# Optimization experiments

Measured on AMD Instinct MI355X. Metric: run time of the kernel, lower is better.

Reference implementation:

```python
import jax, jax.numpy as jnp
import numpy as np

ROT = 8
EPS = 1e-5


def _rot_offsets(ks, r):
    # integer-rounded rotated kernel tap offsets, exactly as cal_rot_pad
    c = (ks - 1) / 2
    locx = np.array([[j - c for j in range(ks)] for _ in range(ks)])
    locy = np.array([[i - c for _ in range(ks)] for i in range(ks)])
    loc = np.concatenate((locx.reshape(-1, 1), locy.reshape(-1, 1)), axis=1)  # [ks*ks, (x,y)]
    offs = []
    for i in range(r):
        th = 2.0 * np.pi / r * i
        R = np.array([[np.cos(th), -np.sin(th)], [np.sin(th), np.cos(th)]])
        offs.append(np.around(loc @ R).astype(np.int64))
    m = int(max(int(o.max()) for o in offs))
    return offs, m


def _build_rot_kernel(w, offs, m, r, separate):
    # w: [oc_r, cin, ks, ks]. The torch per-angle pad+cat+1x1conv+crop equals a
    # zero-padded (2m+1)x(2m+1) conv whose kernel scatters w[o,row,col,cin] at
    # (m - y_rot, m - x_rot), accumulating rounding collisions. Non-separate
    # layers cyclically roll the r input-channel blocks by the rotation index.
    oc_r, cin, ks, _ = w.shape
    K = 2 * m + 1
    kers = []
    for i in range(r):
        if separate:
            wi = w
        else:
            wb = w.reshape(oc_r, r, cin // r, ks, ks)
            wi = jnp.roll(wb, i, axis=1).reshape(oc_r, cin, ks, ks)
        wflat = wi.reshape(oc_r, cin, ks * ks)  # row-major tap order matches offs
        l = offs[i]
        ker = jnp.zeros((oc_r, cin, K, K), w.dtype)
        ker = ker.at[:, :, m - l[:, 1], m - l[:, 0]].add(wflat)
        kers.append(ker)
    return jnp.concatenate(kers, axis=0)  # rotation-major out channels, like torch.cat


def _conv(x, w, pad):
    return jax.lax.conv_general_dilated(
        x, w, (1, 1), [(pad, pad), (pad, pad)],
        dimension_numbers=('NCHW', 'OIHW', 'NCHW'))


def _rot_bn(x, gamma, beta, r):
    # training-mode BN applied independently to each rotation chunk, shared params
    B, C, H, W = x.shape
    xs = x.reshape(B, r, C // r, H, W)
    mu = xs.mean(axis=(0, 3, 4), keepdims=True)
    var = xs.var(axis=(0, 3, 4), keepdims=True)
    xn = (xs - mu) * jax.lax.rsqrt(var + EPS)
    xn = xn * gamma[None, None, :, None, None] + beta[None, None, :, None, None]
    return xn.reshape(B, C, H, W)


def _bn(x, gamma, beta):
    mu = x.mean(axis=(0, 2, 3), keepdims=True)
    var = x.var(axis=(0, 2, 3), keepdims=True)
    return (x - mu) * jax.lax.rsqrt(var + EPS) * gamma[None, :, None, None] + beta[None, :, None, None]


def _max_pool(x, k, pad=0):
    return jax.lax.reduce_window(
        x, -jnp.inf, jax.lax.max, (1, 1, k, k), (1, 1, k, k),
        [(0, 0), (0, 0), (pad, pad), (pad, pad)])


def _nms(x, r):
    # note: view is [B, C/r, r, H, W] (rotation-minor), exactly as the torch code
    B, C, H, W = x.shape
    xs = x.reshape(B, C // r, r, H, W)
    y = jnp.max(xs, axis=2, keepdims=True)
    mask = (y != xs).astype(x.dtype)
    return jnp.mean(xs * mask)


def _forward(x, w1, g1, b1, w2, g2, b2, w3, g3, b3,
             w4, g4, b4, w5, g5, b5, w6, g6, b6, w7, b7):
    offs, m = _rot_offsets(3, ROT)  # m == 1 for 3x3
    out = _conv(x, _build_rot_kernel(w1, offs, m, ROT, True), m)
    out = jax.nn.relu(_rot_bn(out, g1, b1, ROT))
    out = _conv(out, _build_rot_kernel(w2, offs, m, ROT, False), m)
    out = jax.nn.relu(_rot_bn(out, g2, b2, ROT))
    out = _max_pool(out, 2)
    out = _conv(out, _build_rot_kernel(w3, offs, m, ROT, False), m)
    out = jax.nn.relu(_rot_bn(out, g3, b3, ROT))
    n = _nms(out, ROT)
    out = jax.nn.relu(_bn(_conv(out, w4, 1), g4, b4))
    out = _max_pool(out, 2)
    out = jax.nn.relu(_bn(_conv(out, w5, 1), g5, b5))
    out = jax.nn.relu(_bn(_conv(out, w6, 1), g6, b6))
    out = _max_pool(out, 2, pad=1)
    out = _conv(out, w7, 2) + b7[None, :, None, None]
    out = _max_pool(out, out.shape[2])  # global max pool
    return out.reshape(out.shape[0], -1), n


def setup_inputs():
    key = jax.random.key(0)
    ks = jax.random.split(key, 24)
    f = jnp.float32
    d = {}
    d['x'] = jax.random.normal(ks[0], (2048, 1, 28, 28), f)
    wshapes = {'w1': (2, 1, 3, 3), 'w2': (2, 16, 3, 3), 'w3': (4, 16, 3, 3),
               'w4': (32, 32, 3, 3), 'w5': (64, 32, 3, 3), 'w6': (64, 64, 3, 3),
               'w7': (10, 64, 4, 4)}
    i = 1
    for name, sh in wshapes.items():
        d[name] = jax.random.normal(ks[i], sh, f) * 0.05
        i += 1
    bnc = {'1': 2, '2': 2, '3': 4, '4': 32, '5': 64, '6': 64}
    for suf, c in bnc.items():
        d['g' + suf] = 1.0 + 0.1 * jax.random.normal(ks[i], (c,), f)
        d['b' + suf] = 0.1 * jax.random.normal(ks[i + 1], (c,), f)
        i += 2
    d['b7'] = 0.1 * jax.random.normal(ks[i], (10,), f)
    return d


def reference(x, w1, w2, w3, w4, w5, w6, w7, g1, b1, g2, b2, g3, b3,
              g4, b4, g5, b5, g6, b6, b7):
    return _forward(x, w1, g1, b1, w2, g2, b2, w3, g3, b3,
                    w4, g4, b4, w5, g5, b5, w6, g6, b6, w7, b7)
```

## Files before the change

### kernel.cpp

```cpp
#include <hip/hip_runtime.h>

static constexpr int NB = 2048;
static constexpr float SENT = -1e30f;

typedef __attribute__((ext_vector_type(8))) short bf16x8;
typedef __attribute__((ext_vector_type(8))) unsigned short u16x8;
typedef __attribute__((ext_vector_type(4))) float f32x4;

#define ST_ADDR(base, ch, kind, copy) ((base) + (((ch)*4 + (copy))*32 + (kind)*8))

static constexpr int DST[8][9] = {
  {8,7,6,5,4,3,2,1,0},
  {5,8,7,2,4,6,1,0,3},
  {2,5,8,1,4,7,0,3,6},
  {1,2,5,0,4,8,3,6,7},
  {0,1,2,3,4,5,6,7,8},
  {3,0,1,6,4,2,7,8,5},
  {6,3,0,7,4,1,8,5,2},
  {7,6,3,8,4,0,5,2,1},
};

__device__ __forceinline__ unsigned short f2bf(float f){
  unsigned int u = __float_as_uint(f);
  u += 0x7fffu + ((u>>16)&1u);
  return (unsigned short)(u>>16);
}

__device__ __forceinline__ float bf2f(unsigned short h){
  return __uint_as_float((unsigned int)h << 16);
}

__device__ __forceinline__ unsigned int cvtpk(float lo, float hi){
  unsigned int r;
  asm("v_cvt_pk_bf16_f32 %0, %1, %2" : "=v"(r) : "v"(lo), "v"(hi));
  return r;
}

__device__ __forceinline__ unsigned int bnpair(unsigned int w, float a0, float b0, float a1, float b1){
  float vlo = __uint_as_float(w << 16);
  float vhi = __uint_as_float(w & 0xFFFF0000u);
  float r0 = fmaxf(vlo*a0 + b0, 0.f);
  float r1 = fmaxf(vhi*a1 + b1, 0.f);
  return cvtpk(r0, r1);
}

__device__ __forceinline__ float st_read(const float* base, int ch, int kind){
  return base[((ch*4+0)*32 + kind*8)] + base[((ch*4+1)*32 + kind*8)]
       + base[((ch*4+2)*32 + kind*8)] + base[((ch*4+3)*32 + kind*8)];
}

__device__ __forceinline__ int border_cell(int t){
  if (t<16) return t;
  if (t<32) return 240 + (t-16);
  if (t<46) return (t-31)*16;
  return (t-45)*16 + 15;
}

__global__ __launch_bounds__(256) void k_pre(const float* __restrict__ x, const float* __restrict__ w1,
                                             const float* __restrict__ w2, const float* __restrict__ w3,
                                             const float* __restrict__ w4,
                                             const float* __restrict__ w5, const float* __restrict__ w6,
                                             const float* __restrict__ w7,
                                             unsigned short* __restrict__ B2,
                                             unsigned short* __restrict__ B3,
                                             unsigned short* __restrict__ wb4,
                                             unsigned short* __restrict__ wb5, unsigned short* __restrict__ wb6,
                                             unsigned short* __restrict__ Bl,
                                             float* __restrict__ st){
  int blk = blockIdx.x;
  if (blk < 283){
    int i = blk*256 + threadIdx.x;
    if (i < 18432){
      int tap = i/2048, rem = i%2048, oc = rem/32, ci = rem%32;
      wb5[i] = f2bf(w5[(oc*32+ci)*9 + tap]);
    } else if (i < 55296){
      int j = i - 18432;
      int tap = j/4096, rem = j%4096, oc = rem/64, ci = rem%64;
      wb6[j] = f2bf(w6[(oc*64+ci)*9 + tap]);
    } else if (i < 64512){
      int j = i - 55296;
      int tap = j/1024, rem = j%1024, oc = rem/32, ci = rem%32;
      wb4[j] = f2bf(w4[(oc*32+ci)*9 + tap]);
    } else if (i < 67072){
      int j = i - 64512;
      int c = j >> 9;
      int rem = j & 511;
      int o = rem >> 5, k = rem & 31;
      int tap = c*2 + (k>>4);
      int ci = k & 15;
      unsigned short v = 0;
      if (tap <= 8){
        int rot = o>>1, u = o&1;
        int bb = ci>>1, ui = ci&1;
        int wc = (((bb - rot) & 7)<<1) | ui;
        int kk = 0;
        #pragma unroll
        for (int q=0;q<9;q++) if (DST[rot][q]==tap) kk=q;
        v = f2bf(w2[(u*16+wc)*9 + kk]);
      }
      B2[j] = v;
    } else if (i < 72192){
      int j = i - 67072;
      int c = j >> 10;
      int rem = j & 1023;
      int o = rem >> 5, k = rem & 31;
      int tap = c*2 + (k>>4);
      int ci = k & 15;
      unsigned short v = 0;
      if (tap <= 8){
        int rot = o>>2, uh = (o>>1)&1, ul = o&1;
        int bb = ci>>1, ui = ci&1;
        int wc = (((bb - rot) & 7)<<1) | ui;
        int kk = 0;
        #pragma unroll
        for (int q=0;q<9;q++) if (DST[rot][q]==tap) kk=q;
        v = f2bf(w3[uh*288 + (ul*16+wc)*9 + kk]);
      }
      B3[j] = v;
    }
    return;
  }
  if (blk < 1307){
    int i = (blk-283)*256 + threadIdx.x;
    int n = i>>10, k = i&1023;
    int pos16 = k>>6, ci = k&63;
    int r = pos16>>2, c = pos16&3;
    unsigned short v = 0;
    if (n < 250){
      int pos = n/10, o = n - 10*(n/10);
      int py = pos/5, px = pos - 5*(pos/5);
      int ky = r - py + 2, kx = c - px + 2;
      if (ky>=0 && ky<4 && kx>=0 && kx<4) v = f2bf(w7[(o*64+ci)*16 + ky*4 + kx]);
    }
    Bl[i] = v;
    return;
  }
  __shared__ float red[4][32];
  float wa[18];
  #pragma unroll
  for (int i=0;i<18;i++) wa[i] = w1[i];
  float s[16], s2[16];
  #pragma unroll
  for (int o=0;o<16;o++){ s[o]=0.f; s2[o]=0.f; }
  for (int idx = (blk-1307)*256 + threadIdx.x; idx < NB*784; idx += 512*256){
    int b = idx/784, pix = idx-b*784;
    int py = pix/28, px = pix-py*28;
    const float* xb = x + (size_t)b*784;
    float tap[9];
    #pragma unroll
    for (int d=0; d<9; d++){
      int dy = d/3-1, dx = d%3-1;
      int yy = py+dy, xx = px+dx;
      tap[d] = (yy>=0 && yy<28 && xx>=0 && xx<28) ? xb[yy*28+xx] : 0.f;
    }
    #pragma unroll
    for (int rot=0; rot<8; rot++){
      #pragma unroll
      for (int u=0; u<2; u++){
        float y = 0.f;
        #pragma unroll
        for (int k=0; k<9; k++) y += wa[u*9+k]*tap[DST[rot][k]];
        int ci = rot*2+u;
        s[ci] += y; s2[ci] += y*y;
      }
    }
  }
  int wid = threadIdx.x>>6;
  #pragma unroll
  for (int o=0;o<16;o++){
    float a = s[o], b2 = s2[o];
    #pragma unroll
    for (int off=32; off; off>>=1){ a += __shfl_down(a,off); b2 += __shfl_down(b2,off); }
    if ((threadIdx.x&63)==0){ red[wid][o] = a; red[wid][16+o] = b2; }
  }
  __syncthreads();
  if (threadIdx.x < 32){
    float v = red[0][threadIdx.x]+red[1][threadIdx.x]+red[2][threadIdx.x]+red[3][threadIdx.x];
    int ch = threadIdx.x & 15, kind = threadIdx.x >> 4;
    atomicAdd(ST_ADDR(st, ch, kind, blk & 3), v);
  }
}

template<int CI>
__global__ __launch_bounds__(64) void k_coef(const float* __restrict__ stin,
                                             const float* __restrict__ g, const float* __restrict__ be,
                                             float invN, int gmask,
                                             float* __restrict__ cf){
  int i = threadIdx.x;
  if (i < CI){
    float mu = st_read(stin, i, 0)*invN;
    float var = st_read(stin, i, 1)*invN - mu*mu;
    float a = g[i & gmask]*rsqrtf(var + 1e-5f);
    cf[i] = a; cf[CI + i] = be[i & gmask] - mu*a;
  }
}

__global__ __launch_bounds__(256, 2) void k_conv2m(const float* __restrict__ x,
                                                   const float* __restrict__ w1,
                                                   const unsigned short* __restrict__ B2,
                                                   const float* __restrict__ stin,
                                                   const float* __restrict__ g1, const float* __restrict__ b1,
                                                   unsigned short* __restrict__ p2b,
                                                   float* __restrict__ stout){
  __shared__ float smemf[8640];
  __shared__ float cab[32];
  __shared__ float red[4][32];
  unsigned short* Ls = (unsigned short*)smemf;
  float* xs = smemf + 7680;
  float* out2 = smemf;
  int t = threadIdx.x;
  int wid = t>>6, lane = t&63;
  int quad = lane>>4, m = lane&15;
  float wa[18];
  #pragma unroll
  for (int i=0;i<18;i++) wa[i] = w1[i];
  if (t < 16){
    const float invN = 1.f/1605632.f;
    float mu = st_read(stin, t, 0)*invN;
    float var = st_read(stin, t, 1)*invN - mu*mu;
    float a = g1[t&1]*rsqrtf(var + 1e-5f);
    cab[t] = a; cab[16+t] = b1[t&1] - mu*a;
  }
  int b = blockIdx.x;
  for (int i=t; i<960; i+=256){
    int r = i>>5, c = i&31;
    int iy = r-1, ix = c-1;
    xs[i] = (iy>=0 && iy<28 && ix>=0 && ix<28) ? x[(size_t)b*784 + iy*28 + ix] : 0.f;
  }
  for (int i=t; i<3840; i+=256) ((unsigned long long*)Ls)[i] = 0ULL;
  __syncthreads();
  for (int i=t; i<784; i+=256){
    int py = i/28, px = i - 28*(i/28);
    float tap[9];
    #pragma unroll
    for (int d=0; d<9; d++) tap[d] = xs[(py + d/3)*32 + px + d%3];
    float y[16];
    #pragma unroll
    for (int rot=0; rot<8; rot++){
      #pragma unroll
      for (int u=0; u<2; u++){
        float acc1 = 0.f;
        #pragma unroll
        for (int k=0; k<9; k++) acc1 += wa[u*9+k]*tap[DST[rot][k]];
        y[rot*2+u] = acc1;
      }
    }
    unsigned long long pk[4];
    #pragma unroll
    for (int q=0; q<4; q++){
      float4 A = *(const float4*)(cab + q*4);
      float4 Bv = *(const float4*)(cab + 16 + q*4);
      float r0 = fmaxf(y[q*4+0]*A.x + Bv.x, 0.f);
      float r1 = fmaxf(y[q*4+1]*A.y + Bv.y, 0.f);
      float r2 = fmaxf(y[q*4+2]*A.z + Bv.z, 0.f);
      float r3 = fmaxf(y[q*4+3]*A.w + Bv.w, 0.f);
      unsigned int lo = cvtpk(r0, r1);
      unsigned int hi = cvtpk(r2, r3);
      pk[q] = (unsigned long long)lo | ((unsigned long long)hi<<32);
    }
    int cell = (py+1)*32 + px + 1;
    unsigned long long* dstp = (unsigned long long*)(Ls + cell*16);
    dstp[0]=pk[0]; dstp[1]=pk[1]; dstp[2]=pk[2]; dstp[3]=pk[3];
  }
  __syncthreads();
  int jb[13];
  #pragma unroll
  for (int j=0;j<13;j++){
    int mt = wid + 4*j;
    int pos = (mt < 49) ? (mt*16 + m) : 0;
    int py = pos/28, px = pos - 28*py;
    jb[j] = (py*32 + px)*16 + (quad&1)*8;
  }
  f32x4 acc[13];
  #pragma unroll
  for (int j=0;j<13;j++) acc[j] = (f32x4){0.f,0.f,0.f,0.f};
  #pragma unroll
  for (int c=0;c<5;c++){
    const int tapA = 2*c, tapB = (2*c+1 < 9) ? 2*c+1 : 8;
    const int offA = ((tapA/3)*32 + tapA%3)*16;
    const int offB = ((tapB/3)*32 + tapB%3)*16;
    int sel = (quad < 2) ? offA : offB;
    bf16x8 Bf = *(const bf16x8*)(B2 + (c*16 + m)*32 + quad*8);
    #pragma unroll
    for (int j=0;j<13;j++){
      int mt = wid + 4*j;
      if (mt >= 49) continue;
      bf16x8 Af = *(const bf16x8*)(Ls + jb[j] + sel);
      acc[j] = __builtin_amdgcn_mfma_f32_16x16x32_bf16(Af, Bf, acc[j], 0, 0, 0);
    }
  }
  __syncthreads();
  float s = 0.f, sq = 0.f;
  #pragma unroll
  for (int j=0;j<13;j++){
    int mt = wid + 4*j;
    if (mt >= 49) continue;
    #pragma unroll
    for (int p=0;p<2;p++){
      int pos0 = mt*16 + quad*4 + p*2;
      float v0 = acc[j][2*p], v1 = acc[j][2*p+1];
      s += v0 + v1; sq += v0*v0 + v1*v1;
      float hm = fmaxf(v0, v1);
      int py = pos0/28, px2 = (pos0 - py*28)>>1;
      out2[(py*14+px2)*17 + m] = hm;
    }
  }
  s += __shfl_down(s,32);  s += __shfl_down(s,16);
  sq += __shfl_down(sq,32); sq += __shfl_down(sq,16);
  if (lane < 16){ red[wid][m] = s; red[wid][16+m] = sq; }
  __syncthreads();
  if (t < 32){
    float v = red[0][t]+red[1][t]+red[2][t]+red[3][t];
    int ch = t & 15, kind = t >> 4;
    atomicAdd(ST_ADDR(stout, ch, kind, b & 3), v);
  }
  unsigned short* pb = p2b + (size_t)b*4096;
  for (int i=t; i<3136; i+=256){
    int cell = i>>4, oc = i&15;
    int yo = cell/14, xo = cell - yo*14;
    float mx = fmaxf(out2[((2*yo)*14+xo)*17 + oc], out2[((2*yo+1)*14+xo)*17 + oc]);
    pb[((yo+1)*16 + xo + 1)*16 + oc] = f2bf(mx);
  }
  for (int i=t; i<960; i+=256){
    int bc = border_cell(i>>4), oc = i&15;
    pb[bc*16 + oc] = f2bf(SENT);
  }
}

__global__ __launch_bounds__(256, 2) void k_conv3m(const unsigned short* __restrict__ p2b,
                                                   const unsigned short* __restrict__ B3,
                                                   const float* __restrict__ stin,
                                                   const float* __restrict__ g2, const float* __restrict__ b2,
                                                   unsigned short* __restrict__ y3b,
                                                   float* __restrict__ stout){
  __shared__ unsigned short Ls[256*16];
  __shared__ float ca[16], cb[16];
  __shared__ float red[4][64];
  int t = threadIdx.x;
  int wid = t>>6, lane = t&63;
  int quad = lane>>4, m = lane&15;
  int b = blockIdx.x;
  const unsigned short* sb = p2b + (size_t)b*4096;
  uint4 Uw0 = *(const uint4*)(sb + (size_t)t*16);
  uint4 Uw1 = *(const uint4*)(sb + (size_t)t*16 + 8);
  if (t < 16){
    const float invN = 1.f/1605632.f;
    float mu = st_read(stin, t, 0)*invN;
    float var = st_read(stin, t, 1)*invN - mu*mu;
    float a = g2[t&1]*rsqrtf(var + 1e-5f);
    ca[t] = a; cb[t] = b2[t&1] - mu*a;
  }
  __syncthreads();
  {
    unsigned int p0 = bnpair(Uw0.x, ca[0],cb[0], ca[1],cb[1]);
    unsigned int p1 = bnpair(Uw0.y, ca[2],cb[2], ca[3],cb[3]);
    unsigned int p2 = bnpair(Uw0.z, ca[4],cb[4], ca[5],cb[5]);
    unsigned int p3 = bnpair(Uw0.w, ca[6],cb[6], ca[7],cb[7]);
    unsigned int p4 = bnpair(Uw1.x, ca[8],cb[8], ca[9],cb[9]);
    unsigned int p5 = bnpair(Uw1.y, ca[10],cb[10], ca[11],cb[11]);
    unsigned int p6 = bnpair(Uw1.z, ca[12],cb[12], ca[13],cb[13]);
    unsigned int p7 = bnpair(Uw1.w, ca[14],cb[14], ca[15],cb[15]);
    unsigned long long* dstp = (unsigned long long*)(Ls + t*16);
    dstp[0] = (unsigned long long)p0 | ((unsigned long long)p1<<32);
    dstp[1] = (unsigned long long)p2 | ((unsigned long long)p3<<32);
    dstp[2] = (unsigned long long)p4 | ((unsigned long long)p5<<32);
    dstp[3] = (unsigned long long)p6 | ((unsigned long long)p7<<32);
  }
  __syncthreads();
  int jb[4]; bool vt[4];
  #pragma unroll
  for (int j=0;j<4;j++){
    int mt = wid + 4*j;
    int pos = mt*16 + m;
    vt[j] = (mt <= 12);
    if (pos >= 196) pos = 0;
    int py = pos/14, px = pos - 14*(pos/14);
    jb[j] = (py*16 + px)*16 + (quad&1)*8;
  }
  unsigned short* yb = y3b + (size_t)b*8192;
  float sa[2], sqa[2];
  #pragma unroll
  for (int nt=0; nt<2; nt++){
    f32x4 acc[4];
    #pragma unroll
    for (int j=0;j<4;j++) acc[j] = (f32x4){0.f,0.f,0.f,0.f};
    #pragma unroll
    for (int c=0;c<5;c++){
      const int tapA = 2*c, tapB = (2*c+1 < 9) ? 2*c+1 : 8;
      const int offA = ((tapA/3)*16 + tapA%3)*16;
      const int offB = ((tapB/3)*16 + tapB%3)*16;
      int sel = (quad < 2) ? offA : offB;
      bf16x8 Bf = *(const bf16x8*)(B3 + (c*32 + nt*16 + m)*32 + quad*8);
      #pragma unroll
      for (int j=0;j<4;j++){
        if (!vt[j]) continue;
        bf16x8 Af = *(const bf16x8*)(Ls + jb[j] + sel);
        acc[j] = __builtin_amdgcn_mfma_f32_16x16x32_bf16(Af, Bf, acc[j], 0, 0, 0);
      }
    }
    float s = 0.f, sq = 0.f;
    #pragma unroll
    for (int j=0;j<4;j++){
      if (!vt[j]) continue;
      int mt = wid + 4*j;
      #pragma unroll
      for (int r=0;r<4;r++){
        int pos = mt*16 + quad*4 + r;
        if (pos < 196){
          float v = acc[j][r];
          int py2 = pos/14, px2 = pos - py2*14;
          yb[(size_t)((py2+1)*16 + px2 + 1)*32 + nt*16 + m] = f2bf(v);
          s += v; sq += v*v;
        }
      }
    }
    s += __shfl_down(s,32);  s += __shfl_down(s,16);
    sq += __shfl_down(sq,32); sq += __shfl_down(sq,16);
    sa[nt] = s; sqa[nt] = sq;
  }
  if (lane < 16){
    red[wid][m]      = sa[0];  red[wid][32+m]      = sqa[0];
    red[wid][16+m]   = sa[1];  red[wid][32+16+m]   = sqa[1];
  }
  __syncthreads();
  if (t < 64){
    float v = red[0][t]+red[1][t]+red[2][t]+red[3][t];
    int ch = t & 31, kind = t >> 5;
    atomicAdd(ST_ADDR(stout, ch, kind, b & 3), v);
  }
  for (int i=t; i<1920; i+=256){
    int bc = border_cell(i>>5), oc = i&31;
    yb[(size_t)bc*32 + oc] = f2bf(SENT);
  }
}

__global__ __launch_bounds__(256, 2) void k_conv4w(const unsigned short* __restrict__ y3b,
                                                   const unsigned short* __restrict__ wb4,
                                                   const float* __restrict__ stin,
                                                   const float* __restrict__ g3, const float* __restrict__ b3,
                                                   float* __restrict__ p4,
                                                   float* __restrict__ stout,
                                                   float* __restrict__ nmsa){
  __shared__ unsigned short act[4][8192];
  __shared__ float ca[32], cb[32];
  __shared__ float red[4][64];
  int t = threadIdx.x;
  int wid = t>>6, lane = t&63;
  int quad = lane>>4, m = lane&15;
  if (t < 32){
    const float invN = 1.f/401408.f;
    float mu = st_read(stin, t, 0)*invN;
    float var = st_read(stin, t, 1)*invN - mu*mu;
    float a = g3[t&3]*rsqrtf(var + 1e-5f);
    ca[t] = a; cb[t] = b3[t&3] - mu*a;
  }
  __syncthreads();
  int b = blockIdx.x*4 + wid;
  unsigned short* A = act[wid];
  const unsigned short* sb = y3b + (size_t)b*8192;
  #pragma unroll
  for (int k=0;k<4;k++){
    int cell = lane + 64*k;
    const uint4* src = (const uint4*)(sb + cell*32);
    int sw = cell & 3;
    unsigned short* dst = A + cell*32;
    #pragma unroll
    for (int c=0;c<4;c++){
      uint4 W = src[c];
      int c0 = c*8;
      unsigned int q0 = bnpair(W.x, ca[c0+0],cb[c0+0], ca[c0+1],cb[c0+1]);
      unsigned int q1 = bnpair(W.y, ca[c0+2],cb[c0+2], ca[c0+3],cb[c0+3]);
      unsigned int q2 = bnpair(W.z, ca[c0+4],cb[c0+4], ca[c0+5],cb[c0+5]);
      unsigned int q3 = bnpair(W.w, ca[c0+6],cb[c0+6], ca[c0+7],cb[c0+7]);
      unsigned long long* q = (unsigned long long*)(dst + ((c ^ sw)<<3));
      q[0] = (unsigned long long)q0 | ((unsigned long long)q1<<32);
      q[1] = (unsigned long long)q2 | ((unsigned long long)q3<<32);
    }
  }
  asm volatile("s_waitcnt lgkmcnt(0)" ::: "memory");
  __builtin_amdgcn_sched_barrier(0);
  float nloc = 0.f;
  for (int i=lane; i<784; i+=64){
    int hw = i>>2, c4 = i&3;
    int cell = (hw/14 + 1)*16 + hw%14 + 1;
    const unsigned int* g32 = (const unsigned int*)(A + cell*32 + ((c4 ^ (cell&3))<<3));
    unsigned int w0 = g32[0], w1 = g32[1], w2 = g32[2], w3 = g32[3];
    float v[8];
    v[0] = __uint_as_float(w0 << 16); v[1] = __uint_as_float(w0 & 0xFFFF0000u);
    v[2] = __uint_as_float(w1 << 16); v[3] = __uint_as_float(w1 & 0xFFFF0000u);
    v[4] = __uint_as_float(w2 << 16); v[5] = __uint_as_float(w2 & 0xFFFF0000u);
    v[6] = __uint_as_float(w3 << 16); v[7] = __uint_as_float(w3 & 0xFFFF0000u);
    float vmax = -1e30f;
    #pragma unroll
    for (int r=0;r<8;r++) vmax = fmaxf(vmax, v[r]);
    #pragma unroll
    for (int r=0;r<8;r++) nloc += (v[r] != vmax) ? v[r] : 0.f;
  }
  #pragma unroll
  for (int off=32; off; off>>=1) nloc += __shfl_down(nloc, off);
  if (lane == 0) atomicAdd(&nmsa[(b & 7)*32], nloc);
  int jc[13], jp[13];
  #pragma unroll
  for (int j=0;j<13;j++){
    int pos = j*16 + m;
    if (pos >= 196) pos = 0;
    int py = pos/14, px = pos - 14*(pos/14);
    jc[j] = py*16 + px;
    jp[j] = px;
  }
  f32x4 acc[13][2];
  #pragma unroll
  for (int j=0;j<13;j++){ acc[j][0] = (f32x4){0,0,0,0}; acc[j][1] = (f32x4){0,0,0,0}; }
  #pragma unroll
  for (int tap=0; tap<9; tap++){
    const int dy = tap/3, dx = tap - 3*(tap/3);
    bf16x8 Bf0 = *(const bf16x8*)(wb4 + (tap*32 + m)*32 + quad*8);
    bf16x8 Bf1 = *(const bf16x8*)(wb4 + (tap*32 + 16 + m)*32 + quad*8);
    #pragma unroll
    for (int j=0;j<13;j++){
      int ci = jc[j] + dy*16 + dx;
      int ph = quad ^ ((jp[j]+dx)&3);
      bf16x8 Af = *(const bf16x8*)(A + ci*32 + ph*8);
      acc[j][0] = __builtin_amdgcn_mfma_f32_16x16x32_bf16(Af, Bf0, acc[j][0], 0, 0, 0);
      acc[j][1] = __builtin_amdgcn_mfma_f32_16x16x32_bf16(Af, Bf1, acc[j][1], 0, 0, 0);
    }
  }
  asm volatile("s_waitcnt lgkmcnt(0)" ::: "memory");
  __builtin_amdgcn_sched_barrier(0);
  float* hp = (float*)A;
  float s0=0.f, sq0=0.f, s1=0.f, sq1=0.f;
  #pragma unroll
  for (int j=0;j<13;j++){
    #pragma unroll
    for (int p=0;p<2;p++){
      int pos0 = j*16 + quad*4 + 2*p;
      if (pos0 + 1 < 196){
        float a0 = acc[j][0][2*p], a1 = acc[j][0][2*p+1];
        float b0 = acc[j][1][2*p], b1 = acc[j][1][2*p+1];
        s0 += a0 + a1; sq0 += a0*a0 + a1*a1;
        s1 += b0 + b1; sq1 += b0*b0 + b1*b1;
        int py0 = pos0/14, pxh = (pos0 - py0*14)>>1;
        hp[(py0*7 + pxh)*33 + m]      = fmaxf(a0, a1);
        hp[(py0*7 + pxh)*33 + 16 + m] = fmaxf(b0, b1);
      }
    }
  }
  s0 += __shfl_down(s0,32); s0 += __shfl_down(s0,16);
  sq0 += __shfl_down(sq0,32); sq0 += __shfl_down(sq0,16);
  s1 += __shfl_down(s1,32); s1 += __shfl_down(s1,16);
  sq1 += __shfl_down(sq1,32); sq1 += __shfl_down(sq1,16);
  if (lane < 16){
    red[wid][m]      = s0;  red[wid][32+m]      = sq0;
    red[wid][16+m]   = s1;  red[wid][32+16+m]   = sq1;
  }
  asm volatile("s_waitcnt lgkmcnt(0)" ::: "memory");
  __builtin_amdgcn_sched_barrier(0);
  for (int i=lane; i<1568; i+=64){
    int cell = i>>5, oc = i&31;
    int yo = cell/7, xo = cell - yo*7;
    float mx = fmaxf(hp[((2*yo)*7 + xo)*33 + oc], hp[((2*yo+1)*7 + xo)*33 + oc]);
    p4[((size_t)b*49 + cell)*32 + oc] = mx;
  }
  __syncthreads();
  if (t < 64){
    float v = red[0][t]+red[1][t]+red[2][t]+red[3][t];
    int ch = t & 31, kind = t >> 5;
    atomicAdd(ST_ADDR(stout, ch, kind, blockIdx.x & 3), v);
  }
}

template<int CI>
__global__ __launch_bounds__(256, 2) void k_conv56m(const float* __restrict__ src,
                                                    const unsigned short* __restrict__ wb,
                                                    const float* __restrict__ stin,
                                                    const float* __restrict__ g, const float* __restrict__ be,
                                                    float invN,
                                                    float* __restrict__ dst,
                                                    float* __restrict__ stout){
  constexpr int CIP = CI + 8;
  constexpr int KC = CI/32;
  __shared__ unsigned short lin[4][81*CIP];
  __shared__ float red[4][256];
  __shared__ float ca[CI], cb[CI];
  int wid = threadIdx.x>>6, lane = threadIdx.x&63;
  int quad = lane>>4, m = lane&15;
  unsigned short* L = lin[wid];
  if (threadIdx.x < CI){
    int i = threadIdx.x;
    float mu = st_read(stin, i, 0)*invN;
    float var = st_read(stin, i, 1)*invN - mu*mu;
    float a = g[i]*rsqrtf(var + 1e-5f);
    ca[i] = a; cb[i] = be[i] - mu*a;
  }
  for (int i = lane; i < 81*CIP/4; i += 64) ((unsigned long long*)L)[i] = 0ULL;
  __syncthreads();
  int b = blockIdx.x*4 + wid;
  const float* sb = src + (size_t)b*49*CI;
  for (int i = lane; i < 49*CI/4; i += 64){
    int pos = i/(CI/4), cig = i - pos*(CI/4);
    float4 v = *(const float4*)(sb + pos*CI + cig*4);
    float r0 = fmaxf(v.x*ca[cig*4]  +cb[cig*4],   0.f);
    float r1 = fmaxf(v.y*ca[cig*4+1]+cb[cig*4+1], 0.f);
    float r2 = fmaxf(v.z*ca[cig*4+2]+cb[cig*4+2], 0.f);
    float r3 = fmaxf(v.w*ca[cig*4+3]+cb[cig*4+3], 0.f);
    int pos9 = (pos/7 + 1)*9 + pos%7 + 1;
    unsigned int lo = cvtpk(r0, r1);
    unsigned int hi = cvtpk(r2, r3);
    *(unsigned long long*)(L + pos9*CIP + cig*4) =
        (unsigned long long)lo | ((unsigned long long)hi<<32);
  }
  __syncthreads();
  int py[4], px[4];
  #pragma unroll
  for (int mt=0; mt<4; mt++){
    int pos = mt*16 + m;
    if (pos < 49){ py[mt] = pos/7; px[mt] = pos%7; }
    else { py[mt] = 0; px[mt] = 0; }
  }
  f32x4 acc[4][4];
  #pragma unroll
  for (int nt=0; nt<4; nt++)
    #pragma unroll
    for (int mt=0; mt<4; mt++) acc[nt][mt] = (f32x4){0.f,0.f,0.f,0.f};

  for (int tap=0; tap<9; tap++){
    int dy = tap/3, dx = tap - dy*3;
    int o9[4];
    #pragma unroll
    for (int mt=0; mt<4; mt++) o9[mt] = ((py[mt]+dy)*9 + px[mt]+dx)*CIP;
    #pragma unroll
    for (int kc=0; kc<KC; kc++){
      int ko = kc*32 + quad*8;
      bf16x8 Bf[4], Af[4];
      #pragma unroll
      for (int nt=0; nt<4; nt++)
        Bf[nt] = *(const bf16x8*)(wb + (tap*64 + nt*16 + m)*CI + ko);
      #pragma unroll
      for (int mt=0; mt<4; mt++)
        Af[mt] = *(const bf16x8*)(L + o9[mt] + ko);
      #pragma unroll
      for (int nt=0; nt<4; nt++)
        #pragma unroll
        for (int mt=0; mt<4; mt++)
          acc[nt][mt] = __builtin_amdgcn_mfma_f32_16x16x32_bf16(Af[mt], Bf[nt], acc[nt][mt], 0, 0, 0);
    }
  }
  float* db = dst + (size_t)b*49*64;
  float snt[4], sqnt[4];
  #pragma unroll
  for (int nt=0; nt<4; nt++){
    float s = 0.f, sq = 0.f;
    #pragma unroll
    for (int mt=0; mt<4; mt++){
      #pragma unroll
      for (int r=0; r<4; r++){
        int pos = mt*16 + quad*4 + r;
        if (pos < 49){
          float v = acc[nt][mt][r];
          db[pos*64 + nt*16 + m] = v;
          s += v; sq += v*v;
        }
      }
    }
    s += __shfl_down(s, 32);  s += __shfl_down(s, 16);
    sq += __shfl_down(sq, 32); sq += __shfl_down(sq, 16);
    snt[nt] = s; sqnt[nt] = sq;
  }
  if (lane < 16){
    #pragma unroll
    for (int nt=0; nt<4; nt++){
      red[wid][nt*16 + lane] = snt[nt];
      red[wid][128 + nt*16 + lane] = sqnt[nt];
    }
  }
  __syncthreads();
  if (threadIdx.x < 128){
    int c = threadIdx.x & 63;
    int off = (threadIdx.x < 64) ? threadIdx.x : (128 + c);
    float v = red[0][off]+red[1][off]+red[2][off]+red[3][off];
    int kind = (threadIdx.x < 64) ? 0 : 1;
    atomicAdd(ST_ADDR(stout, c, kind, blockIdx.x & 3), v);
  }
}

__global__ __launch_bounds__(256) void k_pool6(const float* __restrict__ y,
                                               const float* __restrict__ cf,
                                               unsigned short* __restrict__ p6b){
  int idx = blockIdx.x*256 + threadIdx.x;
  int oc = idx & 63; int t2 = idx >> 6;
  int xo = t2 & 3;  int yo = (t2>>2) & 3;  int b = t2 >> 4;
  float a = cf[oc];
  float bo = cf[64 + oc];
  const float* src = y + (size_t)b*3136;
  float mx = -1e30f;
  #pragma unroll
  for (int dy=0;dy<2;dy++){
    int iy = yo*2 - 1 + dy;
    if (iy < 0 || iy >= 7) continue;
    #pragma unroll
    for (int dx=0;dx<2;dx++){
      int ix = xo*2 - 1 + dx;
      if (ix < 0 || ix >= 7) continue;
      mx = fmaxf(mx, src[(iy*7+ix)*64 + oc]*a + bo);
    }
  }
  p6b[(size_t)b*1024 + (yo*4 + xo)*64 + oc] = f2bf(fmaxf(mx, 0.f));
}

__global__ __launch_bounds__(256) void k_gemm7(const unsigned short* __restrict__ A,
                                               const unsigned short* __restrict__ Bl,
                                               float* __restrict__ part){
  __shared__ float Lw[4][16*65];
  int wid = threadIdx.x>>6, lane = threadIdx.x&63;
  int quad = lane>>4, m = lane&15;
  int blkm = blockIdx.x >> 2, blkn = blockIdx.x & 3;
  int rowb = blkm*64 + wid*16 + m;
  const unsigned short* Arow = A + (size_t)rowb*1024;
  f32x4 acc[4];
  #pragma unroll
  for (int nt=0; nt<4; nt++) acc[nt] = (f32x4){0.f,0.f,0.f,0.f};
  for (int kc=0; kc<32; kc++){
    bf16x8 Af = *(const bf16x8*)(Arow + kc*32 + quad*8);
    #pragma unroll
    for (int nt=0; nt<4; nt++){
      bf16x8 Bf = *(const bf16x8*)(Bl + (size_t)(blkn*64 + nt*16 + m)*1024 + kc*32 + quad*8);
      acc[nt] = __builtin_amdgcn_mfma_f32_16x16x32_bf16(Af, Bf, acc[nt], 0, 0, 0);
    }
  }
  float* Lp = &Lw[wid][0];
  #pragma unroll
  for (int nt=0; nt<4; nt++)
    #pragma unroll
    for (int r=0; r<4; r++)
      Lp[(quad*4+r)*65 + nt*16 + m] = acc[nt][r];
  __syncthreads();
  for (int i=lane; i<160; i+=64){
    int br = i/10, o = i - 10*(i/10);
    int c0 = ((o - blkn*64) % 10 + 10) % 10;
    float mx = -1e30f;
    for (int c=c0; c<64; c+=10){
      if (blkn*64 + c < 250) mx = fmaxf(mx, Lp[br*65 + c]);
    }
    part[((size_t)(blkm*64 + wid*16 + br)*4 + blkn)*10 + o] = mx;
  }
}

__global__ __launch_bounds__(256) void k_logits(const float* __restrict__ part,
                                                const float* __restrict__ bias,
                                                const float* __restrict__ nmsa,
                                                float* __restrict__ out){
  int idx = blockIdx.x*256 + threadIdx.x;
  int b = idx/10, o = idx - 10*(idx/10);
  const float* p = part + (size_t)b*40 + o;
  float mx = fmaxf(fmaxf(p[0], p[10]), fmaxf(p[20], p[30]));
  out[idx] = mx + bias[o];
  if (blockIdx.x == 0 && threadIdx.x == 0){
    float nm = 0.f;
    #pragma unroll
    for (int cp=0; cp<8; cp++) nm += nmsa[cp*32];
    out[20480] = nm * (1.f/12845056.f);
  }
}

extern "C" void kernel_launch(void* const* d_in, const int* in_sizes, int n_in,
                              void* d_out, int out_size, void* d_ws, size_t ws_size,
                              hipStream_t stream){
  const float* x  = (const float*)d_in[0];
  const float* w1 = (const float*)d_in[1];
  const float* w2 = (const float*)d_in[2];
  const float* w3 = (const float*)d_in[3];
  const float* w4 = (const float*)d_in[4];
  const float* w5 = (const float*)d_in[5];
  const float* w6 = (const float*)d_in[6];
  const float* w7 = (const float*)d_in[7];
  const float* g1 = (const float*)d_in[8];
  const float* b1 = (const float*)d_in[9];
  const float* g2 = (const float*)d_in[10];
  const float* b2 = (const float*)d_in[11];
  const float* g3 = (const float*)d_in[12];
  const float* b3 = (const float*)d_in[13];
  const float* g4 = (const float*)d_in[14];
  const float* b4 = (const float*)d_in[15];
  const float* g5 = (const float*)d_in[16];
  const float* b5 = (const float*)d_in[17];
  const float* g6 = (const float*)d_in[18];
  const float* b6 = (const float*)d_in[19];
  const float* b7 = (const float*)d_in[20];
  float* out = (float*)d_out;
  float* W = (float*)d_ws;

  unsigned short* p2b = (unsigned short*)(W + 15728640);
  unsigned short* y3b = (unsigned short*)(W + 24117248);
  float* p4   = W + 0;
  float* st   = W + 3211264;
  float* nmsa = st + 6*8192;
  float* cf6  = nmsa + 256;
  float* y5   = W + 3407872;
  float* y6   = W + 10223616;
  unsigned short* p6b = (unsigned short*)(W + 16646144);
  unsigned short* wb5 = (unsigned short*)(W + 40894464);
  unsigned short* wb6 = (unsigned short*)(W + 40912896);
  unsigned short* wb4 = (unsigned short*)(W + 40931328);
  unsigned short* Bl = (unsigned short*)(W + 40951808);
  float* part = W + 41082880;
  unsigned short* B2 = (unsigned short*)(W + 41164800);
  unsigned short* B3 = (unsigned short*)(W + 41166080);

  hipMemsetAsync(st, 0, 49536*sizeof(float), stream);

  k_pre<<<1819,256,0,stream>>>(x, w1, w2, w3, w4, w5, w6, w7,
                               B2, B3, wb4, wb5, wb6, Bl, st + 0*8192);

  k_conv2m<<<2048,256,0,stream>>>(x, w1, B2, st + 0*8192, g1, b1, p2b, st + 1*8192);

  k_conv3m<<<2048,256,0,stream>>>(p2b, B3, st + 1*8192, g2, b2, y3b, st + 2*8192);

  k_conv4w<<<512,256,0,stream>>>(y3b, wb4, st + 2*8192, g3, b3, p4, st + 3*8192, nmsa);

  k_conv56m<32><<<512,256,0,stream>>>(p4, wb5, st + 3*8192, g4, b4, 1.f/401408.f, y5, st + 4*8192);

  k_conv56m<64><<<512,256,0,stream>>>(y5, wb6, st + 4*8192, g5, b5, 1.f/100352.f, y6, st + 5*8192);

  k_coef<64><<<1,64,0,stream>>>(st + 5*8192, g6, b6, 1.f/100352.f, 63, cf6);

  k_pool6<<<8192,256,0,stream>>>(y6, cf6, p6b);

  k_gemm7<<<128,256,0,stream>>>(p6b, Bl, part);
  k_logits<<<80,256,0,stream>>>(part, b7, nmsa, out);
}
```

Before: 281.8 us.

## Restructure conv3 to one image per wavefront with padded LDS rows

Conv3 now has each of the four wavefronts in a block process a whole image, launching 512 blocks instead of 2048. Each wave stages its own image in LDS with a 24-element row stride instead of 16, and computes all 13 M-tiles for both N-tiles, so each A fragment load is reused across two MFMAs. The border sentinel writes are vectorised to 32-bit stores. The goal is less per-block overhead, fewer block-wide barriers and better LDS bank spread, at the cost of much higher register pressure (26 accumulators) and fewer blocks to hide latency.

```diff
diff --git a/kernel.cpp b/kernel.cpp
--- a/kernel.cpp
+++ b/kernel.cpp
@@ -327,22 +327,18 @@
   }
 }
 
-__global__ __launch_bounds__(256, 2) void k_conv3m(const unsigned short* __restrict__ p2b,
+__global__ __launch_bounds__(256, 2) void k_conv3w(const unsigned short* __restrict__ p2b,
                                                    const unsigned short* __restrict__ B3,
                                                    const float* __restrict__ stin,
                                                    const float* __restrict__ g2, const float* __restrict__ b2,
                                                    unsigned short* __restrict__ y3b,
                                                    float* __restrict__ stout){
-  __shared__ unsigned short Ls[256*16];
+  __shared__ unsigned short act[4][256*24];
   __shared__ float ca[16], cb[16];
   __shared__ float red[4][64];
   int t = threadIdx.x;
   int wid = t>>6, lane = t&63;
   int quad = lane>>4, m = lane&15;
-  int b = blockIdx.x;
-  const unsigned short* sb = p2b + (size_t)b*4096;
-  uint4 Uw0 = *(const uint4*)(sb + (size_t)t*16);
-  uint4 Uw1 = *(const uint4*)(sb + (size_t)t*16 + 8);
   if (t < 16){
     const float invN = 1.f/1605632.f;
     float mu = st_read(stin, t, 0)*invN;
@@ -351,86 +347,98 @@
     ca[t] = a; cb[t] = b2[t&1] - mu*a;
   }
   __syncthreads();
-  {
-    unsigned int p0 = bnpair(Uw0.x, ca[0],cb[0], ca[1],cb[1]);
-    unsigned int p1 = bnpair(Uw0.y, ca[2],cb[2], ca[3],cb[3]);
-    unsigned int p2 = bnpair(Uw0.z, ca[4],cb[4], ca[5],cb[5]);
-    unsigned int p3 = bnpair(Uw0.w, ca[6],cb[6], ca[7],cb[7]);
-    unsigned int p4 = bnpair(Uw1.x, ca[8],cb[8], ca[9],cb[9]);
-    unsigned int p5 = bnpair(Uw1.y, ca[10],cb[10], ca[11],cb[11]);
-    unsigned int p6 = bnpair(Uw1.z, ca[12],cb[12], ca[13],cb[13]);
-    unsigned int p7 = bnpair(Uw1.w, ca[14],cb[14], ca[15],cb[15]);
-    unsigned long long* dstp = (unsigned long long*)(Ls + t*16);
-    dstp[0] = (unsigned long long)p0 | ((unsigned long long)p1<<32);
-    dstp[1] = (unsigned long long)p2 | ((unsigned long long)p3<<32);
-    dstp[2] = (unsigned long long)p4 | ((unsigned long long)p5<<32);
-    dstp[3] = (unsigned long long)p6 | ((unsigned long long)p7<<32);
-  }
-  __syncthreads();
-  int jb[4]; bool vt[4];
-  #pragma unroll
-  for (int j=0;j<4;j++){
-    int mt = wid + 4*j;
-    int pos = mt*16 + m;
-    vt[j] = (mt <= 12);
+  int b = blockIdx.x*4 + wid;
+  unsigned short* A = act[wid];
+  const unsigned short* sb = p2b + (size_t)b*4096;
+  #pragma unroll
+  for (int k=0;k<4;k++){
+    int cell = lane + 64*k;
+    uint4 U0 = *(const uint4*)(sb + cell*16);
+    uint4 U1 = *(const uint4*)(sb + cell*16 + 8);
+    unsigned int p0 = bnpair(U0.x, ca[0],cb[0], ca[1],cb[1]);
+    unsigned int p1 = bnpair(U0.y, ca[2],cb[2], ca[3],cb[3]);
+    unsigned int p2 = bnpair(U0.z, ca[4],cb[4], ca[5],cb[5]);
+    unsigned int p3 = bnpair(U0.w, ca[6],cb[6], ca[7],cb[7]);
+    unsigned int p4 = bnpair(U1.x, ca[8],cb[8], ca[9],cb[9]);
+    unsigned int p5 = bnpair(U1.y, ca[10],cb[10], ca[11],cb[11]);
+    unsigned int p6 = bnpair(U1.z, ca[12],cb[12], ca[13],cb[13]);
+    unsigned int p7 = bnpair(U1.w, ca[14],cb[14], ca[15],cb[15]);
+    unsigned long long* q = (unsigned long long*)(A + cell*24);
+    q[0] = (unsigned long long)p0 | ((unsigned long long)p1<<32);
+    q[1] = (unsigned long long)p2 | ((unsigned long long)p3<<32);
+    q[2] = (unsigned long long)p4 | ((unsigned long long)p5<<32);
+    q[3] = (unsigned long long)p6 | ((unsigned long long)p7<<32);
+  }
+  asm volatile("s_waitcnt lgkmcnt(0)" ::: "memory");
+  __builtin_amdgcn_sched_barrier(0);
+  int jpix[13];
+  #pragma unroll
+  for (int j=0;j<13;j++){
+    int pos = j*16 + m;
     if (pos >= 196) pos = 0;
     int py = pos/14, px = pos - 14*(pos/14);
-    jb[j] = (py*16 + px)*16 + (quad&1)*8;
-  }
+    jpix[j] = py*16 + px;
+  }
+  f32x4 acc[13][2];
+  #pragma unroll
+  for (int j=0;j<13;j++){ acc[j][0] = (f32x4){0,0,0,0}; acc[j][1] = (f32x4){0,0,0,0}; }
+  int half = (quad&1)*8;
+  #pragma unroll
+  for (int c=0;c<5;c++){
+    const int tapA = 2*c, tapB = (2*c+1 < 9) ? 2*c+1 : 8;
+    const int offA = (tapA/3)*16 + tapA%3;
+    const int offB = (tapB/3)*16 + tapB%3;
+    int sel = (quad < 2) ? offA : offB;
+    bf16x8 Bf0 = *(const bf16x8*)(B3 + (c*32 + m)*32 + quad*8);
+    bf16x8 Bf1 = *(const bf16x8*)(B3 + (c*32 + 16 + m)*32 + quad*8);
+    #pragma unroll
+    for (int j=0;j<13;j++){
+      bf16x8 Af = *(const bf16x8*)(A + (jpix[j] + sel)*24 + half);
+      acc[j][0] = __builtin_amdgcn_mfma_f32_16x16x32_bf16(Af, Bf0, acc[j][0], 0, 0, 0);
+      acc[j][1] = __builtin_amdgcn_mfma_f32_16x16x32_bf16(Af, Bf1, acc[j][1], 0, 0, 0);
+    }
+  }
+  asm volatile("s_waitcnt lgkmcnt(0)" ::: "memory");
+  __builtin_amdgcn_sched_barrier(0);
   unsigned short* yb = y3b + (size_t)b*8192;
-  float sa[2], sqa[2];
-  #pragma unroll
-  for (int nt=0; nt<2; nt++){
-    f32x4 acc[4];
-    #pragma unroll
-    for (int j=0;j<4;j++) acc[j] = (f32x4){0.f,0.f,0.f,0.f};
-    #pragma unroll
-    for (int c=0;c<5;c++){
-      const int tapA = 2*c, tapB = (2*c+1 < 9) ? 2*c+1 : 8;
-      const int offA = ((tapA/3)*16 + tapA%3)*16;
-      const int offB = ((tapB/3)*16 + tapB%3)*16;
-      int sel = (quad < 2) ? offA : offB;
-      bf16x8 Bf = *(const bf16x8*)(B3 + (c*32 + nt*16 + m)*32 + quad*8);
-      #pragma unroll
-      for (int j=0;j<4;j++){
-        if (!vt[j]) continue;
-        bf16x8 Af = *(const bf16x8*)(Ls + jb[j] + sel);
-        acc[j] = __builtin_amdgcn_mfma_f32_16x16x32_bf16(Af, Bf, acc[j], 0, 0, 0);
+  float s0=0.f, sq0=0.f, s1=0.f, sq1=0.f;
+  #pragma unroll
+  for (int j=0;j<13;j++){
+    #pragma unroll
+    for (int r=0;r<4;r++){
+      int pos = j*16 + quad*4 + r;
+      if (pos < 196){
+        float v0 = acc[j][0][r], v1 = acc[j][1][r];
+        int py2 = pos/14, px2 = pos - py2*14;
+        int cell = (py2+1)*16 + px2 + 1;
+        yb[cell*32 + m]      = f2bf(v0);
+        yb[cell*32 + 16 + m] = f2bf(v1);
+        s0 += v0; sq0 += v0*v0; s1 += v1; sq1 += v1*v1;
       }
     }
-    float s = 0.f, sq = 0.f;
-    #pragma unroll
-    for (int j=0;j<4;j++){
-      if (!vt[j]) continue;
-      int mt = wid + 4*j;
-      #pragma unroll
-      for (int r=0;r<4;r++){
-        int pos = mt*16 + quad*4 + r;
-        if (pos < 196){
-          float v = acc[j][r];
-          int py2 = pos/14, px2 = pos - py2*14;
-          yb[(size_t)((py2+1)*16 + px2 + 1)*32 + nt*16 + m] = f2bf(v);
-          s += v; sq += v*v;
-        }
-      }
-    }
-    s += __shfl_down(s,32);  s += __shfl_down(s,16);
-    sq += __shfl_down(sq,32); sq += __shfl_down(sq,16);
-    sa[nt] = s; sqa[nt] = sq;
-  }
+  }
+  {
+    unsigned short sh = f2bf(SENT);
+    unsigned int SP = (unsigned int)sh | ((unsigned int)sh << 16);
+    for (int i=lane; i<960; i+=64){
+      int bc = border_cell(i>>4);
+      int p = i & 15;
+      *(unsigned int*)(yb + bc*32 + p*2) = SP;
+    }
+  }
+  s0 += __shfl_down(s0,32); s0 += __shfl_down(s0,16);
+  sq0 += __shfl_down(sq0,32); sq0 += __shfl_down(sq0,16);
+  s1 += __shfl_down(s1,32); s1 += __shfl_down(s1,16);
+  sq1 += __shfl_down(sq1,32); sq1 += __shfl_down(sq1,16);
   if (lane < 16){
-    red[wid][m]      = sa[0];  red[wid][32+m]      = sqa[0];
-    red[wid][16+m]   = sa[1];  red[wid][32+16+m]   = sqa[1];
+    red[wid][m]      = s0;  red[wid][32+m]      = sq0;
+    red[wid][16+m]   = s1;  red[wid][32+16+m]   = sq1;
   }
   __syncthreads();
   if (t < 64){
     float v = red[0][t]+red[1][t]+red[2][t]+red[3][t];
     int ch = t & 31, kind = t >> 5;
-    atomicAdd(ST_ADDR(stout, ch, kind, b & 3), v);
-  }
-  for (int i=t; i<1920; i+=256){
-    int bc = border_cell(i>>5), oc = i&31;
-    yb[(size_t)bc*32 + oc] = f2bf(SENT);
+    atomicAdd(ST_ADDR(stout, ch, kind, blockIdx.x & 3), v);
   }
 }
 
@@ -813,7 +821,7 @@
 
   k_conv2m<<<2048,256,0,stream>>>(x, w1, B2, st + 0*8192, g1, b1, p2b, st + 1*8192);
 
-  k_conv3m<<<2048,256,0,stream>>>(p2b, B3, st + 1*8192, g2, b2, y3b, st + 2*8192);
+  k_conv3w<<<512,256,0,stream>>>(p2b, B3, st + 1*8192, g2, b2, y3b, st + 2*8192);
 
   k_conv4w<<<512,256,0,stream>>>(y3b, wb4, st + 2*8192, g3, b3, p4, st + 3*8192, nmsa);
 
```

Result: faster. 263.5 us, median of 2 (-6.5%).
